# Kernel tuning notes

Measured on AMD Instinct MI355X. Metric: run time of the kernel, lower is better.

Reference implementation:

```python
import jax, jax.numpy as jnp
import numpy as np

N_TREES = 64
DEPTH = 10           # complete binary trees
ARITY = 2
C = 8                # hidden states
M = 32               # observation labels
G = 8                # n_gen
NPT = 2 ** (DEPTH + 1) - 1   # nodes per tree = 2047
DIM = N_TREES * NPT          # 131008 total nodes


def _levels(parents_cat, children_cat):
    # Static (Python-int) slicing: level d has N_TREES * 2**d children.
    levels, pos = [], 0
    for d in range(1, DEPTH + 1):
        n = N_TREES * (2 ** d)
        levels.append((parents_cat[pos:pos + n], children_cat[pos:pos + n]))
        pos += n
    return levels


def _forward(A, B, Pi, x, roots, leaves, inv_map, trees_ind, parents_cat, children_cat):
    sm_A = jax.nn.softmax(A, axis=0)    # (C,C,G), columns sum to 1 over first axis
    sm_B = jax.nn.softmax(B, axis=1)    # (C,M,G)
    sm_Pi = jax.nn.softmax(Pi, axis=0)  # (C,G)
    log_A, log_Pi = jnp.log(sm_A), jnp.log(sm_Pi)

    levels = _levels(parents_cat, children_cat)
    obs = x[inv_map]
    emit = lambda idx: jnp.transpose(sm_B[:, obs[idx]], (1, 0, 2))  # (n,C,G)

    # ---- preliminary downward: prior[n,i,g] ----
    prior = jnp.zeros((DIM, C, G), dtype=A.dtype)
    prior = prior.at[roots].set(jnp.broadcast_to(sm_Pi, (roots.shape[0], C, G)))
    for pa, ch in levels:
        prior = prior.at[ch].set(jnp.einsum('ijg,njg->nig', sm_A, prior[pa]))

    # ---- upward (beta recursion) ----
    beta = jnp.zeros((DIM, C, G), dtype=A.dtype)
    t_beta = jnp.zeros((DIM, C, G), dtype=A.dtype)
    bl = prior[leaves] * emit(leaves)
    beta = beta.at[leaves].set(bl / bl.sum(1, keepdims=True))
    for pa, ch in reversed(levels):
        ratio = beta[ch] / prior[ch]                       # (n,C,G)
        beta_uv = jnp.einsum('ijg,nig->njg', sm_A, ratio)  # message child->parent
        t_beta = t_beta.at[ch].set(beta_uv)
        u_idx = pa[::ARITY]                                # unique parents (children are contiguous pairs)
        prod_u = beta_uv.reshape(-1, ARITY, C, G).prod(axis=1)  # segmented product over siblings
        bu = prior[u_idx] * emit(u_idx) * prod_u
        beta = beta.at[u_idx].set(bu / bu.sum(1, keepdims=True))

    # ---- downward (eps / t_eps posteriors) ----
    eps = jnp.zeros((DIM, C, G), dtype=A.dtype)
    t_eps = jnp.zeros((DIM, C, C, G), dtype=A.dtype)
    eps = eps.at[roots].set(beta[roots])
    for pa, ch in levels:
        pa_factor = eps[pa][:, None, :, :] * sm_A[None] / t_beta[ch][:, None, :, :]  # (n,C,C,G)
        ch_factor = (beta[ch] / prior[ch])[:, :, None, :]                            # (n,C,1,G)
        te = ch_factor * pa_factor
        t_eps = t_eps.at[ch].set(te)
        num = te.sum(2)
        eps = eps.at[ch].set(num / num.sum(1, keepdims=True))

    # ---- log likelihood, scattered per tree ----
    lik = jnp.zeros((DIM, G), dtype=A.dtype)
    lik = lik.at[roots].add((eps[roots] * log_Pi[None]).sum(1))
    no_root = jnp.concatenate([ch for _, ch in levels])
    lik = lik.at[no_root].add((t_eps[no_root] * log_A[None]).sum((1, 2)))
    internal = jnp.concatenate([pa[::ARITY] for pa, _ in levels])
    all_nodes = jnp.concatenate([internal, leaves])
    lik = lik.at[all_nodes].add((eps[all_nodes] * jnp.log(emit(all_nodes))).sum(1))
    ll = jax.ops.segment_sum(lik, trees_ind, num_segments=N_TREES)  # (N_TREES, G)
    return -ll


def setup_inputs() -> dict:
    key = jax.random.key(0)
    kA, kB, kPi, kx = jax.random.split(key, 4)
    A = jax.random.normal(kA, (C, C, G), dtype=jnp.float32)
    B = jax.random.normal(kB, (C, M, G), dtype=jnp.float32)
    Pi = jax.random.normal(kPi, (C, G), dtype=jnp.float32)
    x = jax.random.randint(kx, (DIM,), 0, M, dtype=jnp.int32)

    offsets = np.arange(N_TREES, dtype=np.int64) * NPT
    parents, children = [], []
    for d in range(1, DEPTH + 1):
        cl = np.arange(2 ** d - 1, 2 ** (d + 1) - 1)   # local child indices at level d
        pl = (cl - 1) // 2                             # local parent indices
        children.append((offsets[:, None] + cl[None, :]).ravel())
        parents.append((offsets[:, None] + pl[None, :]).ravel())
    parents_cat = jnp.asarray(np.concatenate(parents), dtype=jnp.int32)
    children_cat = jnp.asarray(np.concatenate(children), dtype=jnp.int32)
    leaves = jnp.asarray(children[-1], dtype=jnp.int32)
    roots = jnp.asarray(offsets, dtype=jnp.int32)
    inv_map = jnp.arange(DIM, dtype=jnp.int32)
    trees_ind = jnp.asarray(np.repeat(np.arange(N_TREES), NPT), dtype=jnp.int32)
    return {"A": A, "B": B, "Pi": Pi, "x": x, "roots": roots, "leaves": leaves,
            "inv_map": inv_map, "trees_ind": trees_ind,
            "parents_cat": parents_cat, "children_cat": children_cat}


def reference(A, B, Pi, x, roots, leaves, inv_map, trees_ind, parents_cat, children_cat):
    return _forward(A, B, Pi, x, roots, leaves, inv_map, trees_ind, parents_cat, children_cat)
```

## Files before the change

### kernel.cpp

```cpp
#include <hip/hip_runtime.h>


#define NTREES 64
#define DEPTH  10
#define C      8
#define M      32
#define G      8
#define NPT    2047
#define PAD    9
#define BLOCK  512
#define LNODES 1023

__device__ __forceinline__ float frcp(float v) { return __builtin_amdgcn_rcpf(v); }

__device__ __forceinline__ void ldsRead(const float* buf, int node, float (&v)[C]) {
    #pragma unroll
    for (int i = 0; i < C; ++i) v[i] = buf[node*PAD + i];
}
__device__ __forceinline__ void ldsWrite(float* buf, int node, const float (&v)[C]) {
    #pragma unroll
    for (int i = 0; i < C; ++i) buf[node*PAD + i] = v[i];
}

__device__ __forceinline__ void matvec(const float (&sA)[C][C], const float (&p)[C],
                                       float (&o)[C]) {
    #pragma unroll
    for (int i = 0; i < C; ++i) {
        float a = 0.f;
        #pragma unroll
        for (int j = 0; j < C; ++j) a += sA[i][j] * p[j];
        o[i] = a;
    }
}

template<bool ROOT>
__device__ __forceinline__ void up_node(const float (&sA)[C][C], const float (&sB)[C][M],
                                        const float (&rr1)[C], const float (&rr2)[C],
                                        const float (&pr)[C], int xu, float (&outv)[C])
{
    float a1[C], a2[C];
    #pragma unroll
    for (int j = 0; j < C; ++j) { a1[j] = 0.f; a2[j] = 0.f; }
    #pragma unroll
    for (int i = 0; i < C; ++i) {
        #pragma unroll
        for (int j = 0; j < C; ++j) {
            const float aij = sA[i][j];
            a1[j] += aij * rr1[i];
            a2[j] += aij * rr2[i];
        }
    }
    float ep[C]; float Z = 0.f;
    #pragma unroll
    for (int j = 0; j < C; ++j) {
        ep[j] = sB[j][xu] * (a1[j] * a2[j]);
        Z += pr[j] * ep[j];
    }
    const float iz = frcp(Z);
    #pragma unroll
    for (int j = 0; j < C; ++j) outv[j] = ROOT ? pr[j]*ep[j]*iz : ep[j]*iz;
}

template<bool WEPS>
__device__ __forceinline__ float child_node(const float (&sA)[C][C],
                                            const float (&sAL)[C][C],
                                            const float (&lgB)[C][M],
                                            const float (&r)[C],
                                            const float (&epa)[C],
                                            int xv,
                                            float (&eout)[C])
{
    float tb[C];
    #pragma unroll
    for (int j = 0; j < C; ++j) tb[j] = 0.f;
    #pragma unroll
    for (int i = 0; i < C; ++i) {
        #pragma unroll
        for (int j = 0; j < C; ++j) tb[j] += sA[i][j] * r[i];
    }
    float f[C];
    #pragma unroll
    for (int j = 0; j < C; ++j) f[j] = epa[j] * frcp(tb[j]);
    float S = 0.f, likA = 0.f, num[C];
    #pragma unroll
    for (int i = 0; i < C; ++i) {
        float a = 0.f, la = 0.f;
        #pragma unroll
        for (int j = 0; j < C; ++j) { a += sA[i][j] * f[j]; la += sAL[i][j] * f[j]; }
        num[i] = r[i] * a;
        S     += num[i];
        likA  += r[i] * la;
    }
    const float invS = frcp(S);
    float likE = 0.f;
    #pragma unroll
    for (int i = 0; i < C; ++i) {
        const float e2 = num[i] * invS;
        if constexpr (WEPS) eout[i] = e2;
        likE += e2 * lgB[i][xv];
    }
    return likA + likE;
}

__global__ __launch_bounds__(BLOCK, 2)
void htmm_kernel(const float* __restrict__ A,
                 const float* __restrict__ B,
                 const float* __restrict__ Pi,
                 const int*   __restrict__ x,
                 float* __restrict__ out)
{
    __shared__ float buf[LNODES * PAD];
    __shared__ float sA[C][C], sAL[C][C];
    __shared__ float sB[C][M], lgB[C][M];
    __shared__ float spi[C],  lgpi[C];
    __shared__ float bls[C];
    __shared__ float red8[BLOCK / 64];

    const int b   = blockIdx.x;
    const int t   = b >> 3;
    const int g   = b & 7;
    const int tid = threadIdx.x;
    const int base = t * NPT;

    const int s  = 511 + tid;
    const int xs = x[base + s];
    const int x1 = x[base + 2*s + 1];
    const int x2 = x[base + 2*s + 2];

    if (tid < C) {
        const int j = tid;
        float w[C]; float mx = -1e30f;
        #pragma unroll
        for (int i = 0; i < C; ++i) { w[i] = A[(i*C + j)*G + g]; mx = fmaxf(mx, w[i]); }
        float s0 = 0.f; float e[C];
        #pragma unroll
        for (int i = 0; i < C; ++i) { e[i] = expf(w[i] - mx); s0 += e[i]; }
        const float inv = 1.f / s0, ls = logf(s0);
        #pragma unroll
        for (int i = 0; i < C; ++i) {
            const float sm = e[i] * inv;
            sA[i][j]  = sm;
            sAL[i][j] = sm * ((w[i] - mx) - ls);
        }
    } else if (tid == 8) {
        float w[C]; float mx = -1e30f;
        #pragma unroll
        for (int c = 0; c < C; ++c) { w[c] = Pi[c*G + g]; mx = fmaxf(mx, w[c]); }
        float s0 = 0.f; float e[C];
        #pragma unroll
        for (int c = 0; c < C; ++c) { e[c] = expf(w[c] - mx); s0 += e[c]; }
        const float inv = 1.f / s0, ls = logf(s0);
        #pragma unroll
        for (int c = 0; c < C; ++c) { spi[c] = e[c]*inv; lgpi[c] = (w[c]-mx) - ls; }
    } else if (tid >= 64 && tid < 64 + C) {
        const int c = tid - 64;
        float mx = -1e30f;
        #pragma unroll
        for (int m = 0; m < M; ++m) mx = fmaxf(mx, B[(c*M + m)*G + g]);
        float s0 = 0.f;
        #pragma unroll
        for (int m = 0; m < M; ++m) s0 += expf(B[(c*M + m)*G + g] - mx);
        bls[c] = mx + logf(s0);
    }
    __syncthreads();

    if (tid < C * M) {
        const int c = tid >> 5, m = tid & 31;
        const float d0 = B[(c*M + m)*G + g] - bls[c];
        lgB[c][m] = d0;
        sB[c][m]  = expf(d0);
    }
    if (tid == 320) {
        #pragma unroll
        for (int i = 0; i < C; ++i) buf[i] = spi[i];
    }
    __syncthreads();

    #pragma unroll 1
    for (int p = 0; p < 8; p += 2) {
        if (tid < (1 << p)) {
            const int u = (1 << p) - 1 + tid;
            float pp[C], c[C], gk[C];
            ldsRead(buf, u, pp);
            matvec(sA, pp, c);
            matvec(sA, c,  gk);
            const int cb = 2*u + 1, gb = 4*u + 3;
            ldsWrite(buf, cb,   c);  ldsWrite(buf, cb+1, c);
            ldsWrite(buf, gb,   gk); ldsWrite(buf, gb+1, gk);
            ldsWrite(buf, gb+2, gk); ldsWrite(buf, gb+3, gk);
        }
        __syncthreads();
    }

    float ps[C], pc[C];
    {
        const int pas = 255 + (tid >> 1);
        float pp[C];
        ldsRead(buf, pas, pp);
        matvec(sA, pp, ps);
        matvec(sA, ps, pc);
    }
    float rs[C], r1[C], r2[C];
    {
        float Z1 = 0.f, Z2 = 0.f;
        #pragma unroll
        for (int i = 0; i < C; ++i) {
            r1[i] = sB[i][x1]; Z1 += pc[i] * r1[i];
            r2[i] = sB[i][x2]; Z2 += pc[i] * r2[i];
        }
        const float i1 = frcp(Z1), i2 = frcp(Z2);
        #pragma unroll
        for (int i = 0; i < C; ++i) { r1[i] *= i1; r2[i] *= i2; }
        up_node<false>(sA, sB, r1, r2, ps, xs, rs);
        ldsWrite(buf, s, rs);
    }
    __syncthreads();

    #pragma unroll 1
    for (int p = 7; p >= 1; p -= 2) {
        if (tid < (1 << p)) {
            const int u  = (1 << p) - 1 + tid;
            const int c1 = 2*u + 1, c2 = 2*u + 2;
            float rc1[C], rc2[C];
            {
                float ra[C], rb[C], pr[C];
                ldsRead(buf, 2*c1+1, ra); ldsRead(buf, 2*c1+2, rb); ldsRead(buf, c1, pr);
                up_node<false>(sA, sB, ra, rb, pr, x[base + c1], rc1);
            }
            {
                float ra[C], rb[C], pr[C];
                ldsRead(buf, 2*c2+1, ra); ldsRead(buf, 2*c2+2, rb); ldsRead(buf, c2, pr);
                up_node<false>(sA, sB, ra, rb, pr, x[base + c2], rc2);
            }
            float pr[C], ru[C];
            ldsRead(buf, u, pr);
            up_node<false>(sA, sB, rc1, rc2, pr, x[base + u], ru);
            ldsWrite(buf, c1, rc1); ldsWrite(buf, c2, rc2); ldsWrite(buf, u, ru);
        }
        __syncthreads();
    }
    if (tid == 0) {
        float ra[C], rb[C], pr[C], er[C];
        ldsRead(buf, 1, ra); ldsRead(buf, 2, rb); ldsRead(buf, 0, pr);
        up_node<true>(sA, sB, ra, rb, pr, x[base], er);
        ldsWrite(buf, 0, er);
    }
    __syncthreads();

    float lik = 0.f;
    if (tid == 0) {
        const int xr = x[base];
        float er[C];
        ldsRead(buf, 0, er);
        #pragma unroll
        for (int c = 0; c < C; ++c) lik += er[c] * (lgpi[c] + lgB[c][xr]);
    }
    #pragma unroll 1
    for (int q = 1; q <= 7; q += 2) {
        if (tid < (1 << q)) {
            const int v = (1 << q) - 1 + tid, pa = (v - 1) >> 1;
            float epa[C], r[C], ev[C];
            ldsRead(buf, pa, epa);
            ldsRead(buf, v, r);
            lik += child_node<true>(sA, sAL, lgB, r, epa, x[base + v], ev);
            ldsWrite(buf, v, ev);
            const int c1 = 2*v + 1;
            {
                float rc[C], ec[C];
                ldsRead(buf, c1, rc);
                lik += child_node<true>(sA, sAL, lgB, rc, ev, x[base + c1], ec);
                ldsWrite(buf, c1, ec);
            }
            {
                float rc[C], ec[C];
                ldsRead(buf, c1+1, rc);
                lik += child_node<true>(sA, sAL, lgB, rc, ev, x[base + c1 + 1], ec);
                ldsWrite(buf, c1+1, ec);
            }
        }
        __syncthreads();
    }
    {
        const int pas = 255 + (tid >> 1);
        float epa[C], es[C], dummy[C];
        ldsRead(buf, pas, epa);
        lik += child_node<true >(sA, sAL, lgB, rs, epa, xs, es);
        lik += child_node<false>(sA, sAL, lgB, r1, es,  x1, dummy);
        lik += child_node<false>(sA, sAL, lgB, r2, es,  x2, dummy);
    }

    #pragma unroll
    for (int off = 32; off; off >>= 1) lik += __shfl_xor(lik, off, 64);
    if ((tid & 63) == 0) red8[tid >> 6] = lik;
    __syncthreads();
    if (tid == 0) {
        float acc = 0.f;
        #pragma unroll
        for (int w = 0; w < BLOCK/64; ++w) acc += red8[w];
        out[t*G + g] = -acc;
    }
}

extern "C" void kernel_launch(void* const* d_in, const int* in_sizes, int n_in,
                              void* d_out, int out_size, void* d_ws, size_t ws_size,
                              hipStream_t stream) {
    const float* A  = (const float*)d_in[0];
    const float* B  = (const float*)d_in[1];
    const float* Pi = (const float*)d_in[2];
    const int*   x  = (const int*)d_in[3];
    float* out = (float*)d_out;
    htmm_kernel<<<NTREES * G, BLOCK, 0, stream>>>(A, B, Pi, x, out);
}
```

Baseline: 128.5 us.

## Partition tree into per-wavefront subtrees to replace block barriers with wave-local sync

Each of the 8 wavefronts now owns a 255-node subtree below depth 3 and runs its upward and downward passes with only compiler fences instead of block-wide __syncthreads. Only the top 7 nodes use block barriers. Because the trees are complete and level priors are identical across a level, the prior is computed once per depth into a small table rather than per node. This cuts barrier count and prior recomputation, but relies on wavefront-synchronous LDS visibility through an empty asm fence, and many lanes sit idle in the small upper levels of each subtree.

```diff
diff --git a/kernel.cpp b/kernel.cpp
--- a/kernel.cpp
+++ b/kernel.cpp
@@ -2,35 +2,24 @@
 
 
 #define NTREES 64
-#define DEPTH  10
 #define C      8
 #define M      32
 #define G      8
 #define NPT    2047
 #define PAD    9
 #define BLOCK  512
-#define LNODES 1023
+#define SUBN   255
 
 __device__ __forceinline__ float frcp(float v) { return __builtin_amdgcn_rcpf(v); }
-
-__device__ __forceinline__ void ldsRead(const float* buf, int node, float (&v)[C]) {
-    #pragma unroll
-    for (int i = 0; i < C; ++i) v[i] = buf[node*PAD + i];
-}
-__device__ __forceinline__ void ldsWrite(float* buf, int node, const float (&v)[C]) {
-    #pragma unroll
-    for (int i = 0; i < C; ++i) buf[node*PAD + i] = v[i];
-}
-
-__device__ __forceinline__ void matvec(const float (&sA)[C][C], const float (&p)[C],
-                                       float (&o)[C]) {
-    #pragma unroll
-    for (int i = 0; i < C; ++i) {
-        float a = 0.f;
-        #pragma unroll
-        for (int j = 0; j < C; ++j) a += sA[i][j] * p[j];
-        o[i] = a;
-    }
+__device__ __forceinline__ void cfence() { asm volatile("" ::: "memory"); }
+
+__device__ __forceinline__ void ldsRead(const float* p, int slot, float (&v)[C]) {
+    #pragma unroll
+    for (int i = 0; i < C; ++i) v[i] = p[slot*PAD + i];
+}
+__device__ __forceinline__ void ldsWrite(float* p, int slot, const float (&v)[C]) {
+    #pragma unroll
+    for (int i = 0; i < C; ++i) p[slot*PAD + i] = v[i];
 }
 
 template<bool ROOT>
@@ -109,49 +98,49 @@
                  const int*   __restrict__ x,
                  float* __restrict__ out)
 {
-    __shared__ float buf[LNODES * PAD];
+    __shared__ float buf[8 * SUBN * PAD];
+    __shared__ float top[7 * PAD];
     __shared__ float sA[C][C], sAL[C][C];
     __shared__ float sB[C][M], lgB[C][M];
-    __shared__ float spi[C],  lgpi[C];
+    __shared__ float pri[11][C];
+    __shared__ float lgpi[C];
     __shared__ float bls[C];
-    __shared__ float red8[BLOCK / 64];
-
-    const int b   = blockIdx.x;
-    const int t   = b >> 3;
-    const int g   = b & 7;
-    const int tid = threadIdx.x;
+    __shared__ float red8[8];
+
+    const int b    = blockIdx.x;
+    const int t    = b >> 3;
+    const int g    = b & 7;
+    const int tid  = threadIdx.x;
+    const int w    = tid >> 6;
+    const int lane = tid & 63;
     const int base = t * NPT;
-
-    const int s  = 511 + tid;
-    const int xs = x[base + s];
-    const int x1 = x[base + 2*s + 1];
-    const int x2 = x[base + 2*s + 2];
+    const int sbase = w * SUBN;
 
     if (tid < C) {
         const int j = tid;
-        float w[C]; float mx = -1e30f;
-        #pragma unroll
-        for (int i = 0; i < C; ++i) { w[i] = A[(i*C + j)*G + g]; mx = fmaxf(mx, w[i]); }
+        float wv[C]; float mx = -1e30f;
+        #pragma unroll
+        for (int i = 0; i < C; ++i) { wv[i] = A[(i*C + j)*G + g]; mx = fmaxf(mx, wv[i]); }
         float s0 = 0.f; float e[C];
         #pragma unroll
-        for (int i = 0; i < C; ++i) { e[i] = expf(w[i] - mx); s0 += e[i]; }
+        for (int i = 0; i < C; ++i) { e[i] = expf(wv[i] - mx); s0 += e[i]; }
         const float inv = 1.f / s0, ls = logf(s0);
         #pragma unroll
         for (int i = 0; i < C; ++i) {
             const float sm = e[i] * inv;
             sA[i][j]  = sm;
-            sAL[i][j] = sm * ((w[i] - mx) - ls);
+            sAL[i][j] = sm * ((wv[i] - mx) - ls);
         }
     } else if (tid == 8) {
-        float w[C]; float mx = -1e30f;
-        #pragma unroll
-        for (int c = 0; c < C; ++c) { w[c] = Pi[c*G + g]; mx = fmaxf(mx, w[c]); }
+        float wv[C]; float mx = -1e30f;
+        #pragma unroll
+        for (int c = 0; c < C; ++c) { wv[c] = Pi[c*G + g]; mx = fmaxf(mx, wv[c]); }
         float s0 = 0.f; float e[C];
         #pragma unroll
-        for (int c = 0; c < C; ++c) { e[c] = expf(w[c] - mx); s0 += e[c]; }
+        for (int c = 0; c < C; ++c) { e[c] = expf(wv[c] - mx); s0 += e[c]; }
         const float inv = 1.f / s0, ls = logf(s0);
         #pragma unroll
-        for (int c = 0; c < C; ++c) { spi[c] = e[c]*inv; lgpi[c] = (w[c]-mx) - ls; }
+        for (int c = 0; c < C; ++c) { pri[0][c] = e[c]*inv; lgpi[c] = (wv[c]-mx) - ls; }
     } else if (tid >= 64 && tid < 64 + C) {
         const int c = tid - 64;
         float mx = -1e30f;
@@ -170,133 +159,162 @@
         lgB[c][m] = d0;
         sB[c][m]  = expf(d0);
     }
-    if (tid == 320) {
-        #pragma unroll
-        for (int i = 0; i < C; ++i) buf[i] = spi[i];
-    }
-    __syncthreads();
-
-    #pragma unroll 1
-    for (int p = 0; p < 8; p += 2) {
-        if (tid < (1 << p)) {
-            const int u = (1 << p) - 1 + tid;
-            float pp[C], c[C], gk[C];
-            ldsRead(buf, u, pp);
-            matvec(sA, pp, c);
-            matvec(sA, c,  gk);
-            const int cb = 2*u + 1, gb = 4*u + 3;
-            ldsWrite(buf, cb,   c);  ldsWrite(buf, cb+1, c);
-            ldsWrite(buf, gb,   gk); ldsWrite(buf, gb+1, gk);
-            ldsWrite(buf, gb+2, gk); ldsWrite(buf, gb+3, gk);
-        }
-        __syncthreads();
-    }
-
-    float ps[C], pc[C];
+    if (tid == 256) {
+        float p[C], np[C];
+        #pragma unroll
+        for (int c = 0; c < C; ++c) p[c] = pri[0][c];
+        #pragma unroll 1
+        for (int d = 1; d <= 10; ++d) {
+            #pragma unroll
+            for (int i = 0; i < C; ++i) {
+                float a = 0.f;
+                #pragma unroll
+                for (int j = 0; j < C; ++j) a += sA[i][j] * p[j];
+                np[i] = a;
+            }
+            #pragma unroll
+            for (int c = 0; c < C; ++c) { pri[d][c] = np[c]; p[c] = np[c]; }
+        }
+    }
+    __syncthreads();
+
+    int xleaf0, xleaf1;
     {
-        const int pas = 255 + (tid >> 1);
-        float pp[C];
-        ldsRead(buf, pas, pp);
-        matvec(sA, pp, ps);
-        matvec(sA, ps, pc);
-    }
-    float rs[C], r1[C], r2[C];
-    {
-        float Z1 = 0.f, Z2 = 0.f;
-        #pragma unroll
-        for (int i = 0; i < C; ++i) {
-            r1[i] = sB[i][x1]; Z1 += pc[i] * r1[i];
-            r2[i] = sB[i][x2]; Z2 += pc[i] * r2[i];
-        }
-        const float i1 = frcp(Z1), i2 = frcp(Z2);
-        #pragma unroll
-        for (int i = 0; i < C; ++i) { r1[i] *= i1; r2[i] *= i2; }
-        up_node<false>(sA, sB, r1, r2, ps, xs, rs);
-        ldsWrite(buf, s, rs);
-    }
-    __syncthreads();
-
-    #pragma unroll 1
-    for (int p = 7; p >= 1; p -= 2) {
-        if (tid < (1 << p)) {
-            const int u  = (1 << p) - 1 + tid;
-            const int c1 = 2*u + 1, c2 = 2*u + 2;
-            float rc1[C], rc2[C];
-            {
-                float ra[C], rb[C], pr[C];
-                ldsRead(buf, 2*c1+1, ra); ldsRead(buf, 2*c1+2, rb); ldsRead(buf, c1, pr);
-                up_node<false>(sA, sB, ra, rb, pr, x[base + c1], rc1);
-            }
-            {
-                float ra[C], rb[C], pr[C];
-                ldsRead(buf, 2*c2+1, ra); ldsRead(buf, 2*c2+2, rb); ldsRead(buf, c2, pr);
-                up_node<false>(sA, sB, ra, rb, pr, x[base + c2], rc2);
-            }
-            float pr[C], ru[C];
-            ldsRead(buf, u, pr);
-            up_node<false>(sA, sB, rc1, rc2, pr, x[base + u], ru);
-            ldsWrite(buf, c1, rc1); ldsWrite(buf, c2, rc2); ldsWrite(buf, u, ru);
-        }
-        __syncthreads();
-    }
+        const int i0 = lane, q0 = 127 + i0;
+        const int n0 = 1023 + w*128 + i0;
+        xleaf0 = x[base + n0];
+        float rr[C]; float Z = 0.f;
+        #pragma unroll
+        for (int c = 0; c < C; ++c) { rr[c] = sB[c][xleaf0]; Z += pri[10][c] * rr[c]; }
+        const float iz = frcp(Z);
+        #pragma unroll
+        for (int c = 0; c < C; ++c) buf[(sbase+q0)*PAD + c] = rr[c] * iz;
+
+        const int i1 = 64 + lane, q1 = 127 + i1;
+        xleaf1 = x[base + n0 + 64];
+        float rr2[C]; float Z2 = 0.f;
+        #pragma unroll
+        for (int c = 0; c < C; ++c) { rr2[c] = sB[c][xleaf1]; Z2 += pri[10][c] * rr2[c]; }
+        const float iz2 = frcp(Z2);
+        #pragma unroll
+        for (int c = 0; c < C; ++c) buf[(sbase+q1)*PAD + c] = rr2[c] * iz2;
+    }
+    cfence();
+
+    int xup[7];
+    #pragma unroll
+    for (int lam = 6; lam >= 0; --lam) {
+        const int sz = 1 << lam;
+        if (lane < sz) {
+            const int q  = sz - 1 + lane;
+            const int n  = ((1 << (3 + lam)) - 1) + w*sz + lane;
+            const int xv = x[base + n];
+            xup[lam] = xv;
+            float ra[C], rb[C], pr[C], ro[C];
+            ldsRead(buf, sbase + 2*q + 1, ra);
+            ldsRead(buf, sbase + 2*q + 2, rb);
+            #pragma unroll
+            for (int c = 0; c < C; ++c) pr[c] = pri[3 + lam][c];
+            up_node<false>(sA, sB, ra, rb, pr, xv, ro);
+            ldsWrite(buf, sbase + q, ro);
+        }
+        cfence();
+    }
+    __syncthreads();
+
+    float lik = 0.f;
+    if (tid < 4) {
+        float ra[C], rb[C], pr[C], ro[C];
+        ldsRead(buf, (2*tid)*SUBN,     ra);
+        ldsRead(buf, (2*tid + 1)*SUBN, rb);
+        #pragma unroll
+        for (int c = 0; c < C; ++c) pr[c] = pri[2][c];
+        up_node<false>(sA, sB, ra, rb, pr, x[base + 3 + tid], ro);
+        ldsWrite(top, 3 + tid, ro);
+    }
+    __syncthreads();
+    if (tid < 2) {
+        float ra[C], rb[C], pr[C], ro[C];
+        ldsRead(top, 3 + 2*tid, ra);
+        ldsRead(top, 4 + 2*tid, rb);
+        #pragma unroll
+        for (int c = 0; c < C; ++c) pr[c] = pri[1][c];
+        up_node<false>(sA, sB, ra, rb, pr, x[base + 1 + tid], ro);
+        ldsWrite(top, 1 + tid, ro);
+    }
+    __syncthreads();
     if (tid == 0) {
         float ra[C], rb[C], pr[C], er[C];
-        ldsRead(buf, 1, ra); ldsRead(buf, 2, rb); ldsRead(buf, 0, pr);
-        up_node<true>(sA, sB, ra, rb, pr, x[base], er);
-        ldsWrite(buf, 0, er);
-    }
-    __syncthreads();
-
-    float lik = 0.f;
-    if (tid == 0) {
+        ldsRead(top, 1, ra);
+        ldsRead(top, 2, rb);
+        #pragma unroll
+        for (int c = 0; c < C; ++c) pr[c] = pri[0][c];
         const int xr = x[base];
-        float er[C];
-        ldsRead(buf, 0, er);
+        up_node<true>(sA, sB, ra, rb, pr, xr, er);
         #pragma unroll
         for (int c = 0; c < C; ++c) lik += er[c] * (lgpi[c] + lgB[c][xr]);
-    }
-    #pragma unroll 1
-    for (int q = 1; q <= 7; q += 2) {
-        if (tid < (1 << q)) {
-            const int v = (1 << q) - 1 + tid, pa = (v - 1) >> 1;
-            float epa[C], r[C], ev[C];
-            ldsRead(buf, pa, epa);
-            ldsRead(buf, v, r);
-            lik += child_node<true>(sA, sAL, lgB, r, epa, x[base + v], ev);
-            ldsWrite(buf, v, ev);
-            const int c1 = 2*v + 1;
-            {
-                float rc[C], ec[C];
-                ldsRead(buf, c1, rc);
-                lik += child_node<true>(sA, sAL, lgB, rc, ev, x[base + c1], ec);
-                ldsWrite(buf, c1, ec);
-            }
-            {
-                float rc[C], ec[C];
-                ldsRead(buf, c1+1, rc);
-                lik += child_node<true>(sA, sAL, lgB, rc, ev, x[base + c1 + 1], ec);
-                ldsWrite(buf, c1+1, ec);
-            }
-        }
-        __syncthreads();
+        ldsWrite(top, 0, er);
+    }
+    __syncthreads();
+    if (tid < 2) {
+        float r[C], epa[C], eo[C];
+        ldsRead(top, 1 + tid, r);
+        ldsRead(top, 0, epa);
+        lik += child_node<true>(sA, sAL, lgB, r, epa, x[base + 1 + tid], eo);
+        ldsWrite(top, 1 + tid, eo);
+    }
+    __syncthreads();
+    if (tid < 4) {
+        float r[C], epa[C], eo[C];
+        ldsRead(top, 3 + tid, r);
+        ldsRead(top, 1 + (tid >> 1), epa);
+        lik += child_node<true>(sA, sAL, lgB, r, epa, x[base + 3 + tid], eo);
+        ldsWrite(top, 3 + tid, eo);
+    }
+    __syncthreads();
+
+    if (lane == 0) {
+        float r[C], epa[C], eo[C];
+        ldsRead(buf, sbase, r);
+        ldsRead(top, 3 + (w >> 1), epa);
+        lik += child_node<true>(sA, sAL, lgB, r, epa, xup[0], eo);
+        ldsWrite(buf, sbase, eo);
+    }
+    cfence();
+    #pragma unroll
+    for (int lam = 1; lam <= 6; ++lam) {
+        const int sz = 1 << lam;
+        if (lane < sz) {
+            const int q  = sz - 1 + lane;
+            const int pa = (q - 1) >> 1;
+            float r[C], epa[C], eo[C];
+            ldsRead(buf, sbase + q,  r);
+            ldsRead(buf, sbase + pa, epa);
+            lik += child_node<true>(sA, sAL, lgB, r, epa, xup[lam], eo);
+            ldsWrite(buf, sbase + q, eo);
+        }
+        cfence();
     }
     {
-        const int pas = 255 + (tid >> 1);
-        float epa[C], es[C], dummy[C];
-        ldsRead(buf, pas, epa);
-        lik += child_node<true >(sA, sAL, lgB, rs, epa, xs, es);
-        lik += child_node<false>(sA, sAL, lgB, r1, es,  x1, dummy);
-        lik += child_node<false>(sA, sAL, lgB, r2, es,  x2, dummy);
+        float r[C], epa[C], dummy[C];
+        const int q0 = 127 + lane, pa0 = (q0 - 1) >> 1;
+        ldsRead(buf, sbase + q0,  r);
+        ldsRead(buf, sbase + pa0, epa);
+        lik += child_node<false>(sA, sAL, lgB, r, epa, xleaf0, dummy);
+        const int q1 = 191 + lane, pa1 = (q1 - 1) >> 1;
+        ldsRead(buf, sbase + q1,  r);
+        ldsRead(buf, sbase + pa1, epa);
+        lik += child_node<false>(sA, sAL, lgB, r, epa, xleaf1, dummy);
     }
 
     #pragma unroll
     for (int off = 32; off; off >>= 1) lik += __shfl_xor(lik, off, 64);
-    if ((tid & 63) == 0) red8[tid >> 6] = lik;
+    if (lane == 0) red8[w] = lik;
     __syncthreads();
     if (tid == 0) {
         float acc = 0.f;
         #pragma unroll
-        for (int w = 0; w < BLOCK/64; ++w) acc += red8[w];
+        for (int k = 0; k < 8; ++k) acc += red8[k];
         out[t*G + g] = -acc;
     }
 }
```

Result: faster. 123.9 us (-3.5%).
